# Optimization experiments

Hardware: AMD Instinct MI355X
Metric: run time of the kernel (lower is better)

## Reference

```python
import jax, jax.numpy as jnp
import numpy as np

N, F_IN, HEADS, D_HEAD, HID, OUT, E = 50000, 128, 4, 64, 256, 2, 800000
NEG_SLOPE = 0.2


def setup_inputs() -> dict:
    key = jax.random.key(0)
    ks = jax.random.split(key, 12)
    x = jax.random.normal(ks[0], (N, F_IN), dtype=jnp.float32)
    edge_index = jax.random.randint(ks[1], (2, E), 0, N, dtype=jnp.int64)
    s = 0.05
    W_gat = jax.random.normal(ks[2], (F_IN, HEADS * D_HEAD), dtype=jnp.float32) * s
    att_src = jax.random.normal(ks[3], (HEADS, D_HEAD), dtype=jnp.float32) * s
    att_dst = jax.random.normal(ks[4], (HEADS, D_HEAD), dtype=jnp.float32) * s
    b_gat = jnp.zeros((HEADS * D_HEAD,), dtype=jnp.float32)
    W1 = jax.random.normal(ks[5], (HEADS * D_HEAD, HID), dtype=jnp.float32) * s
    b1 = jnp.zeros((HID,), dtype=jnp.float32)
    W2 = jax.random.normal(ks[6], (HID, HID), dtype=jnp.float32) * s
    b2 = jnp.zeros((HID,), dtype=jnp.float32)
    W3 = jax.random.normal(ks[7], (HID, OUT), dtype=jnp.float32) * s
    b3 = jnp.zeros((OUT,), dtype=jnp.float32)
    return {"x": x, "edge_index": edge_index, "W_gat": W_gat, "att_src": att_src,
            "att_dst": att_dst, "b_gat": b_gat, "W1": W1, "b1": b1,
            "W2": W2, "b2": b2, "W3": W3, "b3": b3}


def _gat(x, edge_index, W_gat, att_src, att_dst, b_gat):
    n = x.shape[0]
    loop = jnp.arange(n, dtype=edge_index.dtype)
    src = jnp.concatenate([edge_index[0], loop])  # [E+N] message sources j
    dst = jnp.concatenate([edge_index[1], loop])  # [E+N] message targets i
    h = (x @ W_gat).reshape(n, HEADS, D_HEAD)      # [N,H,D]
    a_s = jnp.einsum('nhd,hd->nh', h, att_src)     # [N,H]
    a_d = jnp.einsum('nhd,hd->nh', h, att_dst)     # [N,H]
    e = a_s[src] + a_d[dst]                        # [E',H]
    e = jax.nn.leaky_relu(e, NEG_SLOPE)
    # per-destination-node softmax over incoming edges (numerically stable)
    emax = jax.ops.segment_max(e, dst, num_segments=n)
    e = jnp.exp(e - emax[dst])
    denom = jax.ops.segment_sum(e, dst, num_segments=n)
    alpha = e / denom[dst]                         # [E',H]
    msg = h[src] * alpha[:, :, None]               # [E',H,D]
    out = jax.ops.segment_sum(msg, dst, num_segments=n)  # [N,H,D]
    return out.reshape(n, HEADS * D_HEAD) + b_gat


def reference(x, edge_index, W_gat, att_src, att_dst, b_gat, W1, b1, W2, b2, W3, b3):
    h = _gat(x, edge_index, W_gat, att_src, att_dst, b_gat)
    h = jax.nn.relu(h @ W1 + b1)
    h = jax.nn.relu(h @ W2 + b2)
    return h @ W3 + b3
```

## Files before the change

kernel.cpp:

```cpp
#include <hip/hip_runtime.h>
#include <math.h>

#define N_NODES 50000
#define NP 50048
#define F_IN 128
#define HD 256
#define HID 256
#define NE 800000
#define CAP 64
#define NEG_SLOPE 0.2f

typedef __attribute__((ext_vector_type(8))) __bf16 bf16x8;
typedef __attribute__((ext_vector_type(4))) __bf16 bf16x4;
typedef __attribute__((ext_vector_type(4))) float f32x4;

#define GLD_LDS16(g, l)                                                      \
    __builtin_amdgcn_global_load_lds(                                        \
        (const __attribute__((address_space(1))) unsigned int*)(g),          \
        (__attribute__((address_space(3))) unsigned int*)(l), 16, 0, 0)

#define PB_INIT 196
#define PB_WG   128
#define PB_W1   256
#define PB_W2   256

__global__ __launch_bounds__(256) void prep_kernel(const float* __restrict__ Wg,
                                                   const float* __restrict__ W1,
                                                   const float* __restrict__ W2,
                                                   __bf16* __restrict__ Wg_t,
                                                   __bf16* __restrict__ W1_t,
                                                   __bf16* __restrict__ W2_t,
                                                   int* __restrict__ cnt,
                                                   unsigned short* __restrict__ bucket) {
    int b = blockIdx.x, t = threadIdx.x;
    if (b < PB_INIT) {
        int n = b * 256 + t;
        if (n < N_NODES) { cnt[n] = 1; bucket[n * CAP] = (unsigned short)n; }
    } else if (b < PB_INIT + PB_WG) {
        int i = (b - PB_INIT) * 256 + t;
        int m = i >> 7, k = i & 127;
        Wg_t[i] = (__bf16)Wg[(size_t)k * HD + m];
    } else if (b < PB_INIT + PB_WG + PB_W1) {
        int i = (b - PB_INIT - PB_WG) * 256 + t;
        int m = i >> 8, k = i & 255;
        W1_t[i] = (__bf16)W1[(size_t)k * HID + m];
    } else {
        int i = (b - PB_INIT - PB_WG - PB_W1) * 256 + t;
        int m = i >> 8, k = i & 255;
        W2_t[i] = (__bf16)W2[(size_t)k * HID + m];
    }
}

__global__ __launch_bounds__(256) void fill_kernel(const int* __restrict__ ew,
                                                   int* cnt,
                                                   unsigned short* __restrict__ bucket) {
    int e = blockIdx.x * 256 + threadIdx.x;
    int hi = ew[2 * e + 1];
    unsigned long long bal = __ballot(hi != 0);
    int src, dst;
    if (bal == 0) { src = ew[2 * e]; dst = ew[2 * NE + 2 * e]; }
    else          { src = ew[e];     dst = ew[NE + e]; }
    int pos = atomicAdd(&cnt[dst], 1);
    if (pos < CAP) bucket[dst * CAP + pos] = (unsigned short)src;
}

__global__ __launch_bounds__(256) void gemm1_attn_kernel(const float* __restrict__ x,
                                                         const __bf16* __restrict__ Bt,
                                                         const float* __restrict__ att_src,
                                                         const float* __restrict__ att_dst,
                                                         __bf16* __restrict__ h,
                                                         float* __restrict__ a_s,
                                                         float* __restrict__ a_d) {
    __shared__ __bf16 As[64 * 32];
    __shared__ __bf16 Bs[256 * 32];
    const int t = threadIdx.x;
    const int lane = t & 63, wv = t >> 6;
    const int lr = lane & 15, q = lane >> 4, lk = q * 8;
    const int col_off = wv * 64;
    const int row0 = blockIdx.x * 64;
    const int sr = t >> 2, sk = (t & 3) * 8;
    const int arow = row0 + sr;
    const bool avalid = arow < N_NODES;

    f32x4 acc[4][4];
#pragma unroll
    for (int r = 0; r < 4; ++r)
#pragma unroll
        for (int c = 0; c < 4; ++c) acc[r][c] = f32x4{0.f, 0.f, 0.f, 0.f};

    for (int k0 = 0; k0 < F_IN; k0 += 32) {
        float4 v0 = {0, 0, 0, 0}, v1 = {0, 0, 0, 0};
        if (avalid) {
            const float* xp = &x[(size_t)arow * F_IN + k0 + sk];
            v0 = *(const float4*)xp;
            v1 = *(const float4*)(xp + 4);
        }
        bf16x8 o;
        o[0] = (__bf16)v0.x; o[1] = (__bf16)v0.y; o[2] = (__bf16)v0.z; o[3] = (__bf16)v0.w;
        o[4] = (__bf16)v1.x; o[5] = (__bf16)v1.y; o[6] = (__bf16)v1.z; o[7] = (__bf16)v1.w;
        *(bf16x8*)&As[sr * 32 + sk] = o;
#pragma unroll
        for (int s = 0; s < 4; ++s) {
            int r = s * 64 + sr;
            GLD_LDS16(&Bt[(size_t)r * F_IN + k0 + sk], &Bs[r * 32 + sk]);
        }
        __syncthreads();
        bf16x8 af[4], bfr[4];
#pragma unroll
        for (int i = 0; i < 4; ++i) {
            af[i]  = *(const bf16x8*)&As[(i * 16 + lr) * 32 + lk];
            bfr[i] = *(const bf16x8*)&Bs[(col_off + i * 16 + lr) * 32 + lk];
        }
#pragma unroll
        for (int r = 0; r < 4; ++r)
#pragma unroll
            for (int c = 0; c < 4; ++c)
                acc[r][c] = __builtin_amdgcn_mfma_f32_16x16x32_bf16(af[r], bfr[c], acc[r][c], 0, 0, 0);
        __syncthreads();
    }

    float asv[4], adv[4];
#pragma unroll
    for (int c = 0; c < 4; ++c) {
        int col = col_off + c * 16 + lr;
        asv[c] = att_src[col];
        adv[c] = att_dst[col];
    }
    float ps[4][4], pd[4][4];
#pragma unroll
    for (int r = 0; r < 4; ++r)
#pragma unroll
        for (int i = 0; i < 4; ++i) { ps[r][i] = 0.f; pd[r][i] = 0.f; }

#pragma unroll
    for (int c = 0; c < 4; ++c) {
        int col = col_off + c * 16 + lr;
#pragma unroll
        for (int r = 0; r < 4; ++r) {
#pragma unroll
            for (int i = 0; i < 4; ++i) {
                int row = row0 + r * 16 + q * 4 + i;
                float v = acc[r][c][i];
                h[(size_t)row * HD + col] = (__bf16)v;
                ps[r][i] += v * asv[c];
                pd[r][i] += v * adv[c];
            }
        }
    }
#pragma unroll
    for (int r = 0; r < 4; ++r)
#pragma unroll
        for (int i = 0; i < 4; ++i) {
#pragma unroll
            for (int m = 1; m < 16; m <<= 1) {
                ps[r][i] += __shfl_xor(ps[r][i], m);
                pd[r][i] += __shfl_xor(pd[r][i], m);
            }
        }
    if (lr == 0) {
#pragma unroll
        for (int r = 0; r < 4; ++r)
#pragma unroll
            for (int i = 0; i < 4; ++i) {
                int row = row0 + r * 16 + q * 4 + i;
                a_s[row * 4 + wv] = ps[r][i];
                a_d[row * 4 + wv] = pd[r][i];
            }
    }
}

__device__ __forceinline__ float lrelu(float v) { return v >= 0.f ? v : NEG_SLOPE * v; }

__global__ __launch_bounds__(256) void gat_aggregate_kernel(const __bf16* __restrict__ h,
                                                            const float* __restrict__ a_s,
                                                            const float* __restrict__ a_d,
                                                            const int* __restrict__ cnt,
                                                            const unsigned short* __restrict__ bucket,
                                                            const float* __restrict__ b_gat,
                                                            __bf16* __restrict__ gat) {
    __shared__ unsigned short s_src[4][64];
    __shared__ float s_alpha[4][64][4];
    int lane = threadIdx.x & 63;
    int wv = threadIdx.x >> 6;
    int n = blockIdx.x * 4 + wv;

    int deg = cnt[n];
    if (deg > CAP) deg = CAP;
    int src = n;
    float4 e = {-1e30f, -1e30f, -1e30f, -1e30f};
    float4 ad = *(const float4*)&a_d[n * 4];
    if (lane < deg) {
        src = bucket[n * CAP + lane];
        float4 as4 = *(const float4*)&a_s[src * 4];
        e.x = lrelu(as4.x + ad.x);
        e.y = lrelu(as4.y + ad.y);
        e.z = lrelu(as4.z + ad.z);
        e.w = lrelu(as4.w + ad.w);
    }
    float4 m = e;
#pragma unroll
    for (int off = 1; off < 64; off <<= 1) {
        m.x = fmaxf(m.x, __shfl_xor(m.x, off));
        m.y = fmaxf(m.y, __shfl_xor(m.y, off));
        m.z = fmaxf(m.z, __shfl_xor(m.z, off));
        m.w = fmaxf(m.w, __shfl_xor(m.w, off));
    }
    float4 wgt = {0, 0, 0, 0};
    if (lane < deg) {
        wgt.x = __expf(e.x - m.x); wgt.y = __expf(e.y - m.y);
        wgt.z = __expf(e.z - m.z); wgt.w = __expf(e.w - m.w);
    }
    float4 s = wgt;
#pragma unroll
    for (int off = 1; off < 64; off <<= 1) {
        s.x += __shfl_xor(s.x, off); s.y += __shfl_xor(s.y, off);
        s.z += __shfl_xor(s.z, off); s.w += __shfl_xor(s.w, off);
    }
    s_src[wv][lane] = (unsigned short)src;
    s_alpha[wv][lane][0] = wgt.x / s.x;
    s_alpha[wv][lane][1] = wgt.y / s.y;
    s_alpha[wv][lane][2] = wgt.z / s.z;
    s_alpha[wv][lane][3] = wgt.w / s.w;
    __syncthreads();

    const int half = lane >> 5;
    const int l32 = lane & 31;
    const int c0 = l32 * 8;
    const int head = l32 >> 3;
    float acc[8];
#pragma unroll
    for (int k = 0; k < 8; ++k) acc[k] = 0.f;

    const int mde = (deg + 1) & ~1;
    int j = 0;
    for (; j + 4 <= mde; j += 4) {
        int j0 = j + half, j1 = j + 2 + half;
        int s0 = s_src[wv][j0], s1 = s_src[wv][j1];
        float a0 = s_alpha[wv][j0][head], a1 = s_alpha[wv][j1][head];
        bf16x8 h0 = *(const bf16x8*)&h[(size_t)s0 * HD + c0];
        bf16x8 h1 = *(const bf16x8*)&h[(size_t)s1 * HD + c0];
#pragma unroll
        for (int k = 0; k < 8; ++k)
            acc[k] += a0 * (float)h0[k] + a1 * (float)h1[k];
    }
    for (; j < mde; j += 2) {
        int j0 = j + half;
        int s0 = s_src[wv][j0];
        float a0 = s_alpha[wv][j0][head];
        bf16x8 h0 = *(const bf16x8*)&h[(size_t)s0 * HD + c0];
#pragma unroll
        for (int k = 0; k < 8; ++k)
            acc[k] += a0 * (float)h0[k];
    }
#pragma unroll
    for (int k = 0; k < 8; ++k) acc[k] += __shfl_xor(acc[k], 32);

    if (half == 0) {
        float4 bg0 = *(const float4*)&b_gat[c0];
        float4 bg1 = *(const float4*)&b_gat[c0 + 4];
        bf16x8 o;
        o[0] = (__bf16)(acc[0] + bg0.x); o[1] = (__bf16)(acc[1] + bg0.y);
        o[2] = (__bf16)(acc[2] + bg0.z); o[3] = (__bf16)(acc[3] + bg0.w);
        o[4] = (__bf16)(acc[4] + bg1.x); o[5] = (__bf16)(acc[5] + bg1.y);
        o[6] = (__bf16)(acc[6] + bg1.z); o[7] = (__bf16)(acc[7] + bg1.w);
        *(bf16x8*)&gat[(size_t)n * HD + c0] = o;
    }
}

__global__ __launch_bounds__(256) void fused_mlp_kernel(const __bf16* __restrict__ A,
                                                        const __bf16* __restrict__ W1t,
                                                        const __bf16* __restrict__ W2t,
                                                        const float* __restrict__ b1,
                                                        const float* __restrict__ b2,
                                                        const float* __restrict__ W3,
                                                        const float* __restrict__ b3,
                                                        float* __restrict__ out) {
    __shared__ __bf16 As[64 * 32];
    __shared__ __bf16 Ws[256 * 32];
    __shared__ __bf16 h1s[8 * 64 * 32];
    __shared__ float s_out[64][2];
    const int t = threadIdx.x;
    const int lane = t & 63, wv = t >> 6;
    const int lr = lane & 15, q = lane >> 4, lk = q * 8;
    const int col_off = wv * 64;
    const int row0 = blockIdx.x * 64;
    const int sr = t >> 2, sk = (t & 3) * 8;

    if (t < 128) ((float*)s_out)[t] = 0.f;

    f32x4 acc[4][4];
#pragma unroll
    for (int r = 0; r < 4; ++r)
#pragma unroll
        for (int c = 0; c < 4; ++c) acc[r][c] = f32x4{0.f, 0.f, 0.f, 0.f};

    for (int k0 = 0; k0 < HD; k0 += 32) {
        GLD_LDS16(&A[(size_t)(row0 + sr) * HD + k0 + sk], &As[sr * 32 + sk]);
#pragma unroll
        for (int s = 0; s < 4; ++s) {
            int r = s * 64 + sr;
            GLD_LDS16(&W1t[(size_t)r * HD + k0 + sk], &Ws[r * 32 + sk]);
        }
        __syncthreads();
        bf16x8 af[4], bfr[4];
#pragma unroll
        for (int i = 0; i < 4; ++i) {
            af[i]  = *(const bf16x8*)&As[(i * 16 + lr) * 32 + lk];
            bfr[i] = *(const bf16x8*)&Ws[(col_off + i * 16 + lr) * 32 + lk];
        }
#pragma unroll
        for (int r = 0; r < 4; ++r)
#pragma unroll
            for (int c = 0; c < 4; ++c)
                acc[r][c] = __builtin_amdgcn_mfma_f32_16x16x32_bf16(af[r], bfr[c], acc[r][c], 0, 0, 0);
        __syncthreads();
    }
#pragma unroll
    for (int c = 0; c < 4; ++c) {
        int col = col_off + c * 16 + lr;
        float bv = b1[col];
        int cb = (col >> 5) * 2048;
        int kk = col & 31;
#pragma unroll
        for (int r = 0; r < 4; ++r)
#pragma unroll
            for (int i = 0; i < 4; ++i) {
                int row = r * 16 + q * 4 + i;
                float v = fmaxf(acc[r][c][i] + bv, 0.f);
                h1s[cb + row * 32 + kk] = (__bf16)v;
                acc[r][c][i] = 0.f;
            }
    }
    __syncthreads();

    for (int k0 = 0; k0 < HID; k0 += 32) {
#pragma unroll
        for (int s = 0; s < 4; ++s) {
            int r = s * 64 + sr;
            GLD_LDS16(&W2t[(size_t)r * HID + k0 + sk], &Ws[r * 32 + sk]);
        }
        __syncthreads();
        const int cb = (k0 >> 5) * 2048;
        bf16x8 af[4], bfr[4];
#pragma unroll
        for (int i = 0; i < 4; ++i) {
            af[i]  = *(const bf16x8*)&h1s[cb + (i * 16 + lr) * 32 + lk];
            bfr[i] = *(const bf16x8*)&Ws[(col_off + i * 16 + lr) * 32 + lk];
        }
#pragma unroll
        for (int r = 0; r < 4; ++r)
#pragma unroll
            for (int c = 0; c < 4; ++c)
                acc[r][c] = __builtin_amdgcn_mfma_f32_16x16x32_bf16(af[r], bfr[c], acc[r][c], 0, 0, 0);
        __syncthreads();
    }

    float b2v[4], w30[4], w31[4];
#pragma unroll
    for (int c = 0; c < 4; ++c) {
        int col = col_off + c * 16 + lr;
        b2v[c] = b2[col];
        w30[c] = W3[col * 2];
        w31[c] = W3[col * 2 + 1];
    }
#pragma unroll
    for (int r = 0; r < 4; ++r) {
#pragma unroll
        for (int i = 0; i < 4; ++i) {
            float o0 = 0.f, o1 = 0.f;
#pragma unroll
            for (int c = 0; c < 4; ++c) {
                float v = fmaxf(acc[r][c][i] + b2v[c], 0.f);
                o0 += v * w30[c];
                o1 += v * w31[c];
            }
#pragma unroll
            for (int m = 1; m < 16; m <<= 1) {
                o0 += __shfl_xor(o0, m);
                o1 += __shfl_xor(o1, m);
            }
            if (lr == 0) {
                int row = r * 16 + q * 4 + i;
                atomicAdd(&s_out[row][0], o0);
                atomicAdd(&s_out[row][1], o1);
            }
        }
    }
    __syncthreads();
    if (t < 128) {
        int row = t >> 1, o = t & 1;
        int g = row0 + row;
        if (g < N_NODES) out[g * 2 + o] = s_out[row][o] + b3[o];
    }
}

extern "C" void kernel_launch(void* const* d_in, const int* in_sizes, int n_in,
                              void* d_out, int out_size, void* d_ws, size_t ws_size,
                              hipStream_t stream) {
    const float* x       = (const float*)d_in[0];
    const int*   ei      = (const int*)d_in[1];
    const float* W_gat   = (const float*)d_in[2];
    const float* att_src = (const float*)d_in[3];
    const float* att_dst = (const float*)d_in[4];
    const float* b_gat   = (const float*)d_in[5];
    const float* W1      = (const float*)d_in[6];
    const float* b1      = (const float*)d_in[7];
    const float* W2      = (const float*)d_in[8];
    const float* b2      = (const float*)d_in[9];
    const float* W3      = (const float*)d_in[10];
    const float* b3      = (const float*)d_in[11];
    float* out = (float*)d_out;

    char* ws = (char*)d_ws;
    __bf16* h_bf   = (__bf16*)ws;  ws += (size_t)NP * HD * 2;
    __bf16* gat_bf = (__bf16*)ws;  ws += (size_t)NP * HD * 2;
    __bf16* Wg_t   = (__bf16*)ws;  ws += (size_t)HD * F_IN * 2;
    __bf16* W1_t   = (__bf16*)ws;  ws += (size_t)HID * HD * 2;
    __bf16* W2_t   = (__bf16*)ws;  ws += (size_t)HID * HID * 2;
    float* a_s     = (float*)ws;   ws += (size_t)NP * 4 * 4;
    float* a_d     = (float*)ws;   ws += (size_t)NP * 4 * 4;
    int* cnt       = (int*)ws;     ws += (size_t)N_NODES * 4;
    unsigned short* bucket = (unsigned short*)ws;
    ws += (size_t)N_NODES * CAP * 2;

    prep_kernel<<<PB_INIT + PB_WG + PB_W1 + PB_W2, 256, 0, stream>>>(
        W_gat, W1, W2, Wg_t, W1_t, W2_t, cnt, bucket);
    fill_kernel<<<NE / 256, 256, 0, stream>>>(ei, cnt, bucket);
    gemm1_attn_kernel<<<NP / 64, 256, 0, stream>>>(x, Wg_t, att_src, att_dst,
                                                   h_bf, a_s, a_d);
    gat_aggregate_kernel<<<N_NODES / 4, 256, 0, stream>>>(h_bf, a_s, a_d, cnt, bucket,
                                                          b_gat, gat_bf);
    fused_mlp_kernel<<<NP / 64, 256, 0, stream>>>(gat_bf, W1_t, W2_t, b1, b2, W3, b3, out);
}
```

Baseline: 253.5 us.

## Merge edge fill into GEMM1 launch, one-wave aggregate blocks, unroll gather by 4

```diff
diff --git a/kernel.cpp b/kernel.cpp
--- a/kernel.cpp
+++ b/kernel.cpp
@@ -9,6 +9,7 @@
 #define NE 800000
 #define CAP 64
 #define NEG_SLOPE 0.2f
+#define G1_BLOCKS (NP / 64)
 
 typedef __attribute__((ext_vector_type(8))) __bf16 bf16x8;
 typedef __attribute__((ext_vector_type(4))) __bf16 bf16x4;
@@ -51,28 +52,31 @@
     }
 }
 
-__global__ __launch_bounds__(256) void fill_kernel(const int* __restrict__ ew,
-                                                   int* cnt,
-                                                   unsigned short* __restrict__ bucket) {
-    int e = blockIdx.x * 256 + threadIdx.x;
-    int hi = ew[2 * e + 1];
-    unsigned long long bal = __ballot(hi != 0);
-    int src, dst;
-    if (bal == 0) { src = ew[2 * e]; dst = ew[2 * NE + 2 * e]; }
-    else          { src = ew[e];     dst = ew[NE + e]; }
-    int pos = atomicAdd(&cnt[dst], 1);
-    if (pos < CAP) bucket[dst * CAP + pos] = (unsigned short)src;
-}
-
-__global__ __launch_bounds__(256) void gemm1_attn_kernel(const float* __restrict__ x,
-                                                         const __bf16* __restrict__ Bt,
-                                                         const float* __restrict__ att_src,
-                                                         const float* __restrict__ att_dst,
-                                                         __bf16* __restrict__ h,
-                                                         float* __restrict__ a_s,
-                                                         float* __restrict__ a_d) {
+__global__ __launch_bounds__(256) void g1_fill_kernel(const float* __restrict__ x,
+                                                      const __bf16* __restrict__ Bt,
+                                                      const float* __restrict__ att_src,
+                                                      const float* __restrict__ att_dst,
+                                                      const int* __restrict__ ew,
+                                                      __bf16* __restrict__ h,
+                                                      float* __restrict__ a_s,
+                                                      float* __restrict__ a_d,
+                                                      int* __restrict__ cnt,
+                                                      unsigned short* __restrict__ bucket) {
     __shared__ __bf16 As[64 * 32];
     __shared__ __bf16 Bs[256 * 32];
+
+    if (blockIdx.x >= G1_BLOCKS) {
+        int e = (blockIdx.x - G1_BLOCKS) * 256 + threadIdx.x;
+        int hi = ew[2 * e + 1];
+        unsigned long long bal = __ballot(hi != 0);
+        int src, dst;
+        if (bal == 0) { src = ew[2 * e]; dst = ew[2 * NE + 2 * e]; }
+        else          { src = ew[e];     dst = ew[NE + e]; }
+        int pos = atomicAdd(&cnt[dst], 1);
+        if (pos < CAP) bucket[dst * CAP + pos] = (unsigned short)src;
+        return;
+    }
+
     const int t = threadIdx.x;
     const int lane = t & 63, wv = t >> 6;
     const int lr = lane & 15, q = lane >> 4, lk = q * 8;
@@ -171,18 +175,17 @@
 
 __device__ __forceinline__ float lrelu(float v) { return v >= 0.f ? v : NEG_SLOPE * v; }
 
-__global__ __launch_bounds__(256) void gat_aggregate_kernel(const __bf16* __restrict__ h,
-                                                            const float* __restrict__ a_s,
-                                                            const float* __restrict__ a_d,
-                                                            const int* __restrict__ cnt,
-                                                            const unsigned short* __restrict__ bucket,
-                                                            const float* __restrict__ b_gat,
-                                                            __bf16* __restrict__ gat) {
-    __shared__ unsigned short s_src[4][64];
-    __shared__ float s_alpha[4][64][4];
-    int lane = threadIdx.x & 63;
-    int wv = threadIdx.x >> 6;
-    int n = blockIdx.x * 4 + wv;
+__global__ __launch_bounds__(64) void gat_aggregate_kernel(const __bf16* __restrict__ h,
+                                                           const float* __restrict__ a_s,
+                                                           const float* __restrict__ a_d,
+                                                           const int* __restrict__ cnt,
+                                                           const unsigned short* __restrict__ bucket,
+                                                           const float* __restrict__ b_gat,
+                                                           __bf16* __restrict__ gat) {
+    __shared__ unsigned short s_src[64];
+    __shared__ float s_alpha[64][4];
+    const int lane = threadIdx.x;
+    const int n = blockIdx.x;
 
     int deg = cnt[n];
     if (deg > CAP) deg = CAP;
@@ -216,11 +219,11 @@
         s.x += __shfl_xor(s.x, off); s.y += __shfl_xor(s.y, off);
         s.z += __shfl_xor(s.z, off); s.w += __shfl_xor(s.w, off);
     }
-    s_src[wv][lane] = (unsigned short)src;
-    s_alpha[wv][lane][0] = wgt.x / s.x;
-    s_alpha[wv][lane][1] = wgt.y / s.y;
-    s_alpha[wv][lane][2] = wgt.z / s.z;
-    s_alpha[wv][lane][3] = wgt.w / s.w;
+    s_src[lane] = (unsigned short)src;
+    s_alpha[lane][0] = wgt.x / s.x;
+    s_alpha[lane][1] = wgt.y / s.y;
+    s_alpha[lane][2] = wgt.z / s.z;
+    s_alpha[lane][3] = wgt.w / s.w;
     __syncthreads();
 
     const int half = lane >> 5;
@@ -233,20 +236,24 @@
 
     const int mde = (deg + 1) & ~1;
     int j = 0;
-    for (; j + 4 <= mde; j += 4) {
-        int j0 = j + half, j1 = j + 2 + half;
-        int s0 = s_src[wv][j0], s1 = s_src[wv][j1];
-        float a0 = s_alpha[wv][j0][head], a1 = s_alpha[wv][j1][head];
+    for (; j + 8 <= mde; j += 8) {
+        int j0 = j + half, j1 = j + 2 + half, j2 = j + 4 + half, j3 = j + 6 + half;
+        int s0 = s_src[j0], s1 = s_src[j1], s2 = s_src[j2], s3 = s_src[j3];
+        float a0 = s_alpha[j0][head], a1 = s_alpha[j1][head];
+        float a2 = s_alpha[j2][head], a3 = s_alpha[j3][head];
         bf16x8 h0 = *(const bf16x8*)&h[(size_t)s0 * HD + c0];
         bf16x8 h1 = *(const bf16x8*)&h[(size_t)s1 * HD + c0];
+        bf16x8 h2 = *(const bf16x8*)&h[(size_t)s2 * HD + c0];
+        bf16x8 h3 = *(const bf16x8*)&h[(size_t)s3 * HD + c0];
 #pragma unroll
         for (int k = 0; k < 8; ++k)
-            acc[k] += a0 * (float)h0[k] + a1 * (float)h1[k];
+            acc[k] += a0 * (float)h0[k] + a1 * (float)h1[k]
+                    + a2 * (float)h2[k] + a3 * (float)h3[k];
     }
     for (; j < mde; j += 2) {
         int j0 = j + half;
-        int s0 = s_src[wv][j0];
-        float a0 = s_alpha[wv][j0][head];
+        int s0 = s_src[j0];
+        float a0 = s_alpha[j0][head];
         bf16x8 h0 = *(const bf16x8*)&h[(size_t)s0 * HD + c0];
 #pragma unroll
         for (int k = 0; k < 8; ++k)
@@ -425,10 +432,9 @@
 
     prep_kernel<<<PB_INIT + PB_WG + PB_W1 + PB_W2, 256, 0, stream>>>(
         W_gat, W1, W2, Wg_t, W1_t, W2_t, cnt, bucket);
-    fill_kernel<<<NE / 256, 256, 0, stream>>>(ei, cnt, bucket);
-    gemm1_attn_kernel<<<NP / 64, 256, 0, stream>>>(x, Wg_t, att_src, att_dst,
-                                                   h_bf, a_s, a_d);
-    gat_aggregate_kernel<<<N_NODES / 4, 256, 0, stream>>>(h_bf, a_s, a_d, cnt, bucket,
-                                                          b_gat, gat_bf);
+    g1_fill_kernel<<<G1_BLOCKS + NE / 256, 256, 0, stream>>>(
+        x, Wg_t, att_src, att_dst, ei, h_bf, a_s, a_d, cnt, bucket);
+    gat_aggregate_kernel<<<N_NODES, 64, 0, stream>>>(h_bf, a_s, a_d, cnt, bucket,
+                                                     b_gat, gat_bf);
     fused_mlp_kernel<<<NP / 64, 256, 0, stream>>>(gat_bf, W1_t, W2_t, b1, b2, W3, b3, out);
 }
```

Result: faster. 240.7 us (-5.1%).
